# Performance work log

Measured on AMD Instinct MI355X. Metric: run time of the kernel, lower is better.

## Reference

```python
import jax, jax.numpy as jnp
import numpy as np

B, D, H, DM, O = 8192, 512, 1024, 2048, 256


def setup_inputs() -> dict:
    key = jax.random.key(0)
    ks = jax.random.split(key, 24)
    def rn(k, shape, scale=1.0):
        return jax.random.normal(k, shape, dtype=jnp.float32) * scale
    w = 0.02  # weight init scale
    return {
        "x":  rn(ks[0], (B, D)),
        "h0": rn(ks[1], (B, H), 0.1), "h1": rn(ks[2], (B, H), 0.1),
        "c0": rn(ks[3], (B, H), 0.1), "c1": rn(ks[4], (B, H), 0.1),
        # Bernoulli keep masks with model_prob=1.0 -> all ones
        "m0": jnp.ones((B, H), jnp.float32), "m1": jnp.ones((B, H), jnp.float32),
        # layer 0 gate weights: in = D + H = 1536
        "Wf0": rn(ks[5], (D + H, H), w), "bf0": jnp.full((H,), 0.01, jnp.float32),
        "Wi0": rn(ks[6], (D + H, H), w), "bi0": jnp.full((H,), 0.01, jnp.float32),
        "Wc0": rn(ks[7], (D + H, H), w), "bc0": jnp.full((H,), 0.01, jnp.float32),
        "Wo0": rn(ks[8], (D + H, H), w), "bo0": jnp.full((H,), 0.01, jnp.float32),
        # layer 1 gate weights: in = H + H = 2048
        "Wf1": rn(ks[9],  (2 * H, H), w), "bf1": jnp.full((H,), 0.01, jnp.float32),
        "Wi1": rn(ks[10], (2 * H, H), w), "bi1": jnp.full((H,), 0.01, jnp.float32),
        "Wc1": rn(ks[11], (2 * H, H), w), "bc1": jnp.full((H,), 0.01, jnp.float32),
        "Wo1": rn(ks[12], (2 * H, H), w), "bo1": jnp.full((H,), 0.01, jnp.float32),
        # output MLP: H -> DM -> O (identity activation per default nn.Sequential())
        "Wm1": rn(ks[13], (H, DM), w), "bm1": jnp.full((DM,), 0.01, jnp.float32),
        "Wm2": rn(ks[14], (DM, O), w), "bm2": jnp.full((O,), 0.01, jnp.float32),
    }


def _lstm_cell(comb, c, Wf, bf, Wi, bi, Wc, bc, Wo, bo):
    # fuse the 4 gate GEMMs into one matmul, then split
    W = jnp.concatenate([Wf, Wi, Wc, Wo], axis=1)      # [in, 4H]
    b = jnp.concatenate([bf, bi, bc, bo])               # [4H]
    g = comb @ W + b                                    # [B, 4H]
    f, i, ct, o = jnp.split(g, 4, axis=1)
    c_new = jax.nn.sigmoid(f) * c + jax.nn.sigmoid(i) * jnp.tanh(ct)
    h_new = jax.nn.sigmoid(o) * jnp.tanh(c_new)
    return h_new, c_new


def reference(x, h0, h1, c0, c1, m0, m1,
              Wf0, bf0, Wi0, bi0, Wc0, bc0, Wo0, bo0,
              Wf1, bf1, Wi1, bi1, Wc1, bc1, Wo1, bo1,
              Wm1, bm1, Wm2, bm2):
    # layer 0: combined = cat(input, h0 * mask0)
    comb0 = jnp.concatenate([x, h0 * m0], axis=1)       # [B, D+H]
    h0n, c0n = _lstm_cell(comb0, c0, Wf0, bf0, Wi0, bi0, Wc0, bc0, Wo0, bo0)
    # layer 1: combined = cat(h0_new * mask0, h1 * mask1)
    comb1 = jnp.concatenate([h0n * m0, h1 * m1], axis=1)  # [B, 2H]
    h1n, c1n = _lstm_cell(comb1, c1, Wf1, bf1, Wi1, bi1, Wc1, bc1, Wo1, bo1)
    # output MLP (dropout p=0 is identity; activation is identity Sequential)
    out = (h1n @ Wm1 + bm1) @ Wm2 + bm2                 # [B, O]
    return out, h0n, h1n, c0n, c1n
```

## Files before the change

### kernel.cpp

```cpp
#include <hip/hip_runtime.h>
#include <hip/hip_bf16.h>
#include <cstdint>
#include <cstddef>

#define DI __device__ __forceinline__

typedef __attribute__((ext_vector_type(8))) short short8;
typedef __attribute__((ext_vector_type(4))) float f32x4;

static constexpr int Bb = 8192, Dd = 512, Hh = 1024;

DI short f2b(float f) {
  union { __hip_bfloat16 h; short s; } u;
  u.h = __float2bfloat16(f);
  return u.s;
}

DI float sigm(float x) {
  float e = __builtin_amdgcn_exp2f(-1.4426950408889634f * x);
  return __builtin_amdgcn_rcpf(1.0f + e);
}
DI float tanh_(float x) {
  float xc = fminf(fmaxf(x, -20.0f), 20.0f);
  float e = __builtin_amdgcn_exp2f(-2.8853900817779268f * xc);
  return (1.0f - e) * __builtin_amdgcn_rcpf(1.0f + e);
}

DI void gload16(const void* g, void* l) {
  __builtin_amdgcn_global_load_lds(
      (const __attribute__((address_space(1))) uint32_t*)g,
      (__attribute__((address_space(3))) uint32_t*)l, 16, 0, 0);
}


__global__ void conv_A0(const float* __restrict__ x, const float* __restrict__ h0,
                        const float* __restrict__ m0, short* __restrict__ A0) {
  const int row = blockIdx.x, t = threadIdx.x;
  float v[8];
  if (t < 64) {
    const float4* p = (const float4*)(x + (size_t)row * Dd + t * 8);
    float4 a = p[0], b = p[1];
    v[0] = a.x; v[1] = a.y; v[2] = a.z; v[3] = a.w;
    v[4] = b.x; v[5] = b.y; v[6] = b.z; v[7] = b.w;
  } else {
    const int j = t * 8 - 512;
    const float4* ph = (const float4*)(h0 + (size_t)row * Hh + j);
    const float4* pm = (const float4*)(m0 + (size_t)row * Hh + j);
    float4 a = ph[0], b = ph[1], ma = pm[0], mb = pm[1];
    v[0] = a.x * ma.x; v[1] = a.y * ma.y; v[2] = a.z * ma.z; v[3] = a.w * ma.w;
    v[4] = b.x * mb.x; v[5] = b.y * mb.y; v[6] = b.z * mb.z; v[7] = b.w * mb.w;
  }
  short8 o;
  #pragma unroll
  for (int q = 0; q < 8; q++) o[q] = f2b(v[q]);
  *(short8*)(A0 + (size_t)row * 1536 + t * 8) = o;
}

__global__ void conv_A1hi(const float* __restrict__ h1, const float* __restrict__ m1,
                          short* __restrict__ A1) {
  const int row = blockIdx.x, t = threadIdx.x;
  const int j = t * 8;
  const float4* ph = (const float4*)(h1 + (size_t)row * Hh + j);
  const float4* pm = (const float4*)(m1 + (size_t)row * Hh + j);
  float4 a = ph[0], b = ph[1], ma = pm[0], mb = pm[1];
  float v[8] = {a.x * ma.x, a.y * ma.y, a.z * ma.z, a.w * ma.w,
                b.x * mb.x, b.y * mb.y, b.z * mb.z, b.w * mb.w};
  short8 o;
  #pragma unroll
  for (int q = 0; q < 8; q++) o[q] = f2b(v[q]);
  *(short8*)(A1 + (size_t)row * 2048 + 1024 + j) = o;
}

__global__ void transpose_conv(const float* __restrict__ src, short* __restrict__ dst,
                               int N, int K, int g, int interleave) {
  __shared__ float t[64][65];
  const int k0 = blockIdx.x * 64, n0 = blockIdx.y * 64;
  const int tid = threadIdx.x;
  const int r = tid >> 2, c0 = (tid & 3) * 16;
  const float* s = src + (size_t)(k0 + r) * N + n0 + c0;
  #pragma unroll
  for (int q = 0; q < 16; q += 4) {
    float4 v = *(const float4*)(s + q);
    t[r][c0 + q + 0] = v.x; t[r][c0 + q + 1] = v.y;
    t[r][c0 + q + 2] = v.z; t[r][c0 + q + 3] = v.w;
  }
  __syncthreads();
  const int n = n0 + r;
  const int j = interleave ? ((n >> 4) * 64 + g * 16 + (n & 15)) : n;
  short8 o0, o1;
  #pragma unroll
  for (int q = 0; q < 8; q++) o0[q] = f2b(t[c0 + q][r]);
  #pragma unroll
  for (int q = 0; q < 8; q++) o1[q] = f2b(t[c0 + 8 + q][r]);
  short* d = dst + (size_t)j * K + k0 + c0;
  *(short8*)d = o0;
  *((short8*)d + 1) = o1;
}

__global__ void conv_plain(const float* __restrict__ src, short* __restrict__ dst, int n8) {
  const int id = blockIdx.x * blockDim.x + threadIdx.x;
  if (id >= n8) return;
  const float4* p = (const float4*)(src + (size_t)id * 8);
  float4 a = p[0], b = p[1];
  short8 o;
  o[0] = f2b(a.x); o[1] = f2b(a.y); o[2] = f2b(a.z); o[3] = f2b(a.w);
  o[4] = f2b(b.x); o[5] = f2b(b.y); o[6] = f2b(b.z); o[7] = f2b(b.w);
  *(short8*)(dst + (size_t)id * 8) = o;
}

__global__ void bp_init(const float* __restrict__ bm2, float* __restrict__ bp) {
  bp[threadIdx.x] = bm2[threadIdx.x];
}
__global__ void bp_acc(const float* __restrict__ bm1, const float* __restrict__ Wm2,
                       float* __restrict__ bp) {
  const int o = threadIdx.x;
  const int k0 = blockIdx.x * 64;
  float s = 0.f;
  #pragma unroll 4
  for (int k = 0; k < 64; k++) s += bm1[k0 + k] * Wm2[(size_t)(k0 + k) * 256 + o];
  atomicAdd(&bp[o], s);
}

template <int EPI>
__global__ __launch_bounds__(256) void gemm_bt(
    const short* __restrict__ A, const short* __restrict__ Bt, int K,
    short* __restrict__ Cb, int ldc,
    float* __restrict__ outp, const float* __restrict__ bpv) {
  __shared__ __align__(16) short sA[128 * 32];
  __shared__ __align__(16) short sB[128 * 32];
  const int tid = threadIdx.x;
  const int lane = tid & 63;
  const int wave = tid >> 6;
  const int wm = wave >> 1, wn = wave & 1;
  const int bm = blockIdx.x, bn = blockIdx.y;
  const int lr = lane & 15, lq = lane >> 4;

  f32x4 acc[4][4] = {};

  const short* pA = A + ((size_t)(bm * 128 + (tid >> 2))) * K + (tid & 3) * 8;
  const short* pB = Bt + ((size_t)(bn * 128 + (tid >> 2))) * K + (tid & 3) * 8;
  short* lA = sA + tid * 8;
  short* lB = sB + tid * 8;
  const int aoff = (wm * 64 + lr) * 32 + lq * 8;
  const int boff = (wn * 64 + lr) * 32 + lq * 8;

  for (int k0 = 0; k0 < K; k0 += 32) {
    gload16(pA + k0, lA);
    gload16(pA + (size_t)64 * K + k0, lA + 2048);
    gload16(pB + k0, lB);
    gload16(pB + (size_t)64 * K + k0, lB + 2048);
    __syncthreads();
    short8 af[4], bv[4];
    #pragma unroll
    for (int m = 0; m < 4; m++) af[m] = *(const short8*)&sA[aoff + m * 512];
    #pragma unroll
    for (int n = 0; n < 4; n++) bv[n] = *(const short8*)&sB[boff + n * 512];
    #pragma unroll
    for (int m = 0; m < 4; m++)
      #pragma unroll
      for (int n = 0; n < 4; n++)
        acc[m][n] = __builtin_amdgcn_mfma_f32_16x16x32_bf16(af[m], bv[n], acc[m][n], 0, 0, 0);
    __syncthreads();
  }

  const int crow0 = bm * 128 + wm * 64 + lq * 4;
  const int ccol0 = bn * 128 + wn * 64 + lr;

  if constexpr (EPI == 0) {
    #pragma unroll
    for (int m = 0; m < 4; m++)
      #pragma unroll
      for (int r = 0; r < 4; r++) {
        const int row = crow0 + m * 16 + r;
        #pragma unroll
        for (int n = 0; n < 4; n++)
          Cb[(size_t)row * ldc + ccol0 + n * 16] = f2b(acc[m][n][r]);
      }
  } else {
    float bvv[4];
    #pragma unroll
    for (int n = 0; n < 4; n++) bvv[n] = bpv[ccol0 + n * 16];
    #pragma unroll
    for (int m = 0; m < 4; m++)
      #pragma unroll
      for (int r = 0; r < 4; r++) {
        const int row = crow0 + m * 16 + r;
        #pragma unroll
        for (int n = 0; n < 4; n++)
          outp[(size_t)row * 256 + ccol0 + n * 16] = acc[m][n][r] + bvv[n];
      }
  }
}


#define STA(buf, h, kt) { const short* s_ = gA + (size_t)(h) * 64 * K + (size_t)(kt) * 64; \
    gload16(s_ + aS0, &sA[buf][h][tid * 8]);                                               \
    gload16(s_ + aS1, &sA[buf][h][4096 + tid * 8]); }
#define STB(buf, h, kt) { const short* s_ = gB + (size_t)(h) * 128 * K + (size_t)(kt) * 64; \
    gload16(s_ + bS0, &sB[buf][h][tid * 8]);                                                \
    gload16(s_ + bS1, &sB[buf][h][4096 + tid * 8]); }

#define LDB(buf) {                                                \
    const short* bb = &sB[buf][bh][brb];                          \
    _Pragma("unroll") for (int n = 0; n < 4; n++) {               \
      bv[n][0] = *(const short8*)(bb + n * 1024 + sw0);           \
      bv[n][1] = *(const short8*)(bb + n * 1024 + sw1); } }

#define LDA_(buf, q, av) {                                        \
    const short* ab = &sA[buf][(q) >> 1][arb + ((q) & 1) * 2048]; \
    av[0][0] = *(const short8*)(ab + sw0);                        \
    av[0][1] = *(const short8*)(ab + sw1);                        \
    av[1][0] = *(const short8*)(ab + 1024 + sw0);                 \
    av[1][1] = *(const short8*)(ab + 1024 + sw1); }

#define MM(q, av) {                                               \
    __builtin_amdgcn_s_setprio(1);                                \
    _Pragma("unroll") for (int m = 0; m < 2; m++)                 \
    _Pragma("unroll") for (int n = 0; n < 4; n++) {               \
      acc[2*(q)+m][n] = __builtin_amdgcn_mfma_f32_16x16x32_bf16(av[m][0], bv[n][0], acc[2*(q)+m][n], 0, 0, 0); \
      acc[2*(q)+m][n] = __builtin_amdgcn_mfma_f32_16x16x32_bf16(av[m][1], bv[n][1], acc[2*(q)+m][n], 0, 0, 0); } \
    __builtin_amdgcn_s_setprio(0); }

#define BAR() asm volatile("s_barrier" ::: "memory")
#define VM6() asm volatile("s_waitcnt vmcnt(6)" ::: "memory")

#define PH(buf, q, STG, vm) { short8 av[2][2]; LDA_(buf, q, av); STG; \
    if (vm) VM6(); BAR(); MM(q, av); BAR(); }

__global__ __launch_bounds__(512, 2) void gemm8_lstm(
    const short* __restrict__ A, const short* __restrict__ Bt, const int K,
    const float* __restrict__ cprev, float* __restrict__ hout,
    float* __restrict__ cout, short* __restrict__ anext, const int ldan,
    const float* __restrict__ mask,
    const float* __restrict__ bF, const float* __restrict__ bI,
    const float* __restrict__ bC, const float* __restrict__ bO) {
  __shared__ __align__(16) short sA[2][2][8192];
  __shared__ __align__(16) short sB[2][2][8192];
  const int tid = threadIdx.x;
  const int lane = tid & 63, wid = tid >> 6;
  const int wr = wid >> 2, wc = wid & 3;
  const int lr = lane & 15, lq = lane >> 4;

  const int wgf = blockIdx.y * 32 + blockIdx.x;
  const int swz = (wgf & 7) * 64 + (wgf >> 3);
  const int bm = swz & 31;
  const int bn = swz >> 5;

  const int NT = K >> 6;
  const int NIT = NT >> 1;

  const int r0 = tid >> 3;
  const int csw = (tid & 7) ^ (r0 & 7);
  const int growA0 = ((r0 >> 5) & 1) * 32 + (r0 & 31);
  const int growA1 = 128 + growA0;
  const size_t aS0 = (size_t)growA0 * K + csw * 8;
  const size_t aS1 = (size_t)growA1 * K + csw * 8;
  const size_t bS0 = (size_t)r0 * K + csw * 8;
  const size_t bS1 = (size_t)(r0 + 64) * K + csw * 8;
  const short* gA = A + (size_t)bm * 256 * K;
  const short* gB = Bt + (size_t)bn * 256 * K;

  const int arb = (wr * 64 + lr) * 64;
  const int brb = ((wc & 1) * 64 + lr) * 64;
  const int bh = wc >> 1;
  const int sw0 = ((lq) ^ (lr & 7)) * 8;
  const int sw1 = ((4 + lq) ^ (lr & 7)) * 8;

  f32x4 acc[8][4] = {};
  short8 bv[4][2];

  STB(0, 0, 0); STB(0, 1, 0); STA(0, 0, 0); STA(0, 1, 0);
  STB(1, 0, 1); STB(1, 1, 1); STA(1, 0, 1);
  VM6(); BAR();

  for (int it = 0; it < NIT; ++it) {
    const int k1 = 2 * it + 1;
    int t2 = 2 * it + 2; if (t2 >= NT) t2 = 0;
    int t3 = 2 * it + 3; if (t3 >= NT) t3 = 1;
    { short8 av[2][2]; LDB(0); LDA_(0, 0, av); STA(1, 1, k1); BAR(); MM(0, av); BAR(); }
    PH(0, 1, STB(0, 0, t2), 0);
    PH(0, 2, STB(0, 1, t2), 0);
    PH(0, 3, STA(0, 0, t2), 1);
    { short8 av[2][2]; LDB(1); LDA_(1, 0, av); STA(0, 1, t2); BAR(); MM(0, av); BAR(); }
    PH(1, 1, STB(1, 0, t3), 0);
    PH(1, 2, STB(1, 1, t3), 0);
    PH(1, 3, STA(1, 0, t3), 1);
  }

  const int n = (bn * 4 + wc) * 16 + lr;
  const float bf_ = bF[n], bi_ = bI[n], bc_ = bC[n], bo_ = bO[n];
  const int row0 = bm * 256 + wr * 128 + lq * 4;

  float cp[4], mk[4], cpn[4], mkn[4];
  #pragma unroll
  for (int rr = 0; rr < 4; rr++) {
    const size_t idx = (size_t)(row0 + rr) * 1024 + n;
    cp[rr] = cprev[idx];
    mk[rr] = mask ? mask[idx] : 1.0f;
  }
  #pragma unroll
  for (int mf = 0; mf < 8; mf++) {
    if (mf < 7) {
      #pragma unroll
      for (int rr = 0; rr < 4; rr++) {
        const size_t idx2 = (size_t)(row0 + (mf + 1) * 16 + rr) * 1024 + n;
        cpn[rr] = cprev[idx2];
        mkn[rr] = mask ? mask[idx2] : 1.0f;
      }
    }
    #pragma unroll
    for (int rr = 0; rr < 4; rr++) {
      const int row = row0 + mf * 16 + rr;
      const size_t idx = (size_t)row * 1024 + n;
      const float fg = sigm(acc[mf][0][rr] + bf_);
      const float ig = sigm(acc[mf][1][rr] + bi_);
      const float cg = tanh_(acc[mf][2][rr] + bc_);
      const float og = sigm(acc[mf][3][rr] + bo_);
      const float cn = fg * cp[rr] + ig * cg;
      const float hn = og * tanh_(cn);
      cout[idx] = cn;
      hout[idx] = hn;
      anext[(size_t)row * ldan + n] = f2b(hn * mk[rr]);
    }
    #pragma unroll
    for (int rr = 0; rr < 4; rr++) { cp[rr] = cpn[rr]; mk[rr] = mkn[rr]; }
  }
}


extern "C" void kernel_launch(void* const* d_in, const int* in_sizes, int n_in,
                              void* d_out, int out_size, void* d_ws, size_t ws_size,
                              hipStream_t stream) {
  (void)in_sizes; (void)n_in; (void)out_size; (void)ws_size;
  const float* x   = (const float*)d_in[0];
  const float* h0  = (const float*)d_in[1];
  const float* h1  = (const float*)d_in[2];
  const float* c0  = (const float*)d_in[3];
  const float* c1  = (const float*)d_in[4];
  const float* m0  = (const float*)d_in[5];
  const float* m1  = (const float*)d_in[6];
  const float* Wf0 = (const float*)d_in[7];  const float* bf0 = (const float*)d_in[8];
  const float* Wi0 = (const float*)d_in[9];  const float* bi0 = (const float*)d_in[10];
  const float* Wc0 = (const float*)d_in[11]; const float* bc0 = (const float*)d_in[12];
  const float* Wo0 = (const float*)d_in[13]; const float* bo0 = (const float*)d_in[14];
  const float* Wf1 = (const float*)d_in[15]; const float* bf1 = (const float*)d_in[16];
  const float* Wi1 = (const float*)d_in[17]; const float* bi1 = (const float*)d_in[18];
  const float* Wc1 = (const float*)d_in[19]; const float* bc1 = (const float*)d_in[20];
  const float* Wo1 = (const float*)d_in[21]; const float* bo1 = (const float*)d_in[22];
  const float* Wm1 = (const float*)d_in[23]; const float* bm1 = (const float*)d_in[24];
  const float* Wm2 = (const float*)d_in[25]; const float* bm2 = (const float*)d_in[26];

  float* dout  = (float*)d_out;
  float* out_o = dout;
  float* h0n   = dout + 2097152;
  float* h1n   = h0n + 8388608;
  float* c0n   = h1n + 8388608;
  float* c1n   = c0n + 8388608;

  char* ws = (char*)d_ws;
  short* A0   = (short*)(ws);
  short* A1   = (short*)(ws + 25165824);
  short* A2   = (short*)(ws + 58720256);
  short* WT0  = (short*)(ws + 75497472);
  short* WT1  = (short*)(ws + 88080384);
  short* Wm1b = (short*)(ws + 104857600);
  short* Wm2T = (short*)(ws + 109051904);
  short* WpT  = (short*)(ws + 110100480);
  float* bp   = (float*)(ws + 110624768);

  conv_A0<<<dim3(8192), dim3(192), 0, stream>>>(x, h0, m0, A0);
  conv_A1hi<<<dim3(8192), dim3(128), 0, stream>>>(h1, m1, A1);
  transpose_conv<<<dim3(24, 16), dim3(256), 0, stream>>>(Wf0, WT0, 1024, 1536, 0, 1);
  transpose_conv<<<dim3(24, 16), dim3(256), 0, stream>>>(Wi0, WT0, 1024, 1536, 1, 1);
  transpose_conv<<<dim3(24, 16), dim3(256), 0, stream>>>(Wc0, WT0, 1024, 1536, 2, 1);
  transpose_conv<<<dim3(24, 16), dim3(256), 0, stream>>>(Wo0, WT0, 1024, 1536, 3, 1);
  transpose_conv<<<dim3(32, 16), dim3(256), 0, stream>>>(Wf1, WT1, 1024, 2048, 0, 1);
  transpose_conv<<<dim3(32, 16), dim3(256), 0, stream>>>(Wi1, WT1, 1024, 2048, 1, 1);
  transpose_conv<<<dim3(32, 16), dim3(256), 0, stream>>>(Wc1, WT1, 1024, 2048, 2, 1);
  transpose_conv<<<dim3(32, 16), dim3(256), 0, stream>>>(Wo1, WT1, 1024, 2048, 3, 1);
  conv_plain<<<dim3(1024), dim3(256), 0, stream>>>(Wm1, Wm1b, 262144);
  transpose_conv<<<dim3(32, 4), dim3(256), 0, stream>>>(Wm2, Wm2T, 256, 2048, 0, 0);
  bp_init<<<dim3(1), dim3(256), 0, stream>>>(bm2, bp);
  bp_acc<<<dim3(32), dim3(256), 0, stream>>>(bm1, Wm2, bp);

  gemm_bt<0><<<dim3(2, 8), dim3(256), 0, stream>>>(
      Wm2T, Wm1b, 2048, WpT, 1024, nullptr, nullptr);

  gemm8_lstm<<<dim3(32, 16), dim3(512), 0, stream>>>(
      A0, WT0, 1536, c0, h0n, c0n, A1, 2048, m0, bf0, bi0, bc0, bo0);

  gemm8_lstm<<<dim3(32, 16), dim3(512), 0, stream>>>(
      A1, WT1, 2048, c1, h1n, c1n, A2, 1024, nullptr, bf1, bi1, bc1, bo1);

  gemm_bt<1><<<dim3(64, 2), dim3(256), 0, stream>>>(
      A2, WpT, 1024, nullptr, 0, out_o, bp);
}
```

Baseline: 409.3 us.

## Batch gate-weight transposes into single launches and drop LSTM GEMM block swizzle

Replaces eight per-gate weight transpose launches with two launches that use a z grid dimension to select the gate, cutting launch overhead and small-grid tail effects. The LSTM GEMM kernel also drops its workgroup-index swizzle and maps blockIdx directly to tile row and column, which changes L2 reuse of A and B tiles across concurrently running blocks. The swizzle removal may reduce cache locality.

```diff
diff --git a/kernel.cpp b/kernel.cpp
--- a/kernel.cpp
+++ b/kernel.cpp
@@ -71,8 +71,37 @@
   *(short8*)(A1 + (size_t)row * 2048 + 1024 + j) = o;
 }
 
+__global__ void transpose_conv4(const float* __restrict__ s0, const float* __restrict__ s1,
+                                const float* __restrict__ s2, const float* __restrict__ s3,
+                                short* __restrict__ dst, int N, int K) {
+  __shared__ float t[64][65];
+  const int g = blockIdx.z;
+  const float* src = (g == 0) ? s0 : (g == 1) ? s1 : (g == 2) ? s2 : s3;
+  const int k0 = blockIdx.x * 64, n0 = blockIdx.y * 64;
+  const int tid = threadIdx.x;
+  const int r = tid >> 2, c0 = (tid & 3) * 16;
+  const float* s = src + (size_t)(k0 + r) * N + n0 + c0;
+  #pragma unroll
+  for (int q = 0; q < 16; q += 4) {
+    float4 v = *(const float4*)(s + q);
+    t[r][c0 + q + 0] = v.x; t[r][c0 + q + 1] = v.y;
+    t[r][c0 + q + 2] = v.z; t[r][c0 + q + 3] = v.w;
+  }
+  __syncthreads();
+  const int n = n0 + r;
+  const int j = (n >> 4) * 64 + g * 16 + (n & 15);
+  short8 o0, o1;
+  #pragma unroll
+  for (int q = 0; q < 8; q++) o0[q] = f2b(t[c0 + q][r]);
+  #pragma unroll
+  for (int q = 0; q < 8; q++) o1[q] = f2b(t[c0 + 8 + q][r]);
+  short* d = dst + (size_t)j * K + k0 + c0;
+  *(short8*)d = o0;
+  *((short8*)d + 1) = o1;
+}
+
 __global__ void transpose_conv(const float* __restrict__ src, short* __restrict__ dst,
-                               int N, int K, int g, int interleave) {
+                               int N, int K) {
   __shared__ float t[64][65];
   const int k0 = blockIdx.x * 64, n0 = blockIdx.y * 64;
   const int tid = threadIdx.x;
@@ -86,13 +115,12 @@
   }
   __syncthreads();
   const int n = n0 + r;
-  const int j = interleave ? ((n >> 4) * 64 + g * 16 + (n & 15)) : n;
   short8 o0, o1;
   #pragma unroll
   for (int q = 0; q < 8; q++) o0[q] = f2b(t[c0 + q][r]);
   #pragma unroll
   for (int q = 0; q < 8; q++) o1[q] = f2b(t[c0 + 8 + q][r]);
-  short* d = dst + (size_t)j * K + k0 + c0;
+  short* d = dst + (size_t)n * K + k0 + c0;
   *(short8*)d = o0;
   *((short8*)d + 1) = o1;
 }
@@ -241,10 +269,7 @@
   const int wr = wid >> 2, wc = wid & 3;
   const int lr = lane & 15, lq = lane >> 4;
 
-  const int wgf = blockIdx.y * 32 + blockIdx.x;
-  const int swz = (wgf & 7) * 64 + (wgf >> 3);
-  const int bm = swz & 31;
-  const int bn = swz >> 5;
+  const int bm = blockIdx.x, bn = blockIdx.y;
 
   const int NT = K >> 6;
   const int NIT = NT >> 1;
@@ -370,16 +395,10 @@
 
   conv_A0<<<dim3(8192), dim3(192), 0, stream>>>(x, h0, m0, A0);
   conv_A1hi<<<dim3(8192), dim3(128), 0, stream>>>(h1, m1, A1);
-  transpose_conv<<<dim3(24, 16), dim3(256), 0, stream>>>(Wf0, WT0, 1024, 1536, 0, 1);
-  transpose_conv<<<dim3(24, 16), dim3(256), 0, stream>>>(Wi0, WT0, 1024, 1536, 1, 1);
-  transpose_conv<<<dim3(24, 16), dim3(256), 0, stream>>>(Wc0, WT0, 1024, 1536, 2, 1);
-  transpose_conv<<<dim3(24, 16), dim3(256), 0, stream>>>(Wo0, WT0, 1024, 1536, 3, 1);
-  transpose_conv<<<dim3(32, 16), dim3(256), 0, stream>>>(Wf1, WT1, 1024, 2048, 0, 1);
-  transpose_conv<<<dim3(32, 16), dim3(256), 0, stream>>>(Wi1, WT1, 1024, 2048, 1, 1);
-  transpose_conv<<<dim3(32, 16), dim3(256), 0, stream>>>(Wc1, WT1, 1024, 2048, 2, 1);
-  transpose_conv<<<dim3(32, 16), dim3(256), 0, stream>>>(Wo1, WT1, 1024, 2048, 3, 1);
+  transpose_conv4<<<dim3(24, 16, 4), dim3(256), 0, stream>>>(Wf0, Wi0, Wc0, Wo0, WT0, 1024, 1536);
+  transpose_conv4<<<dim3(32, 16, 4), dim3(256), 0, stream>>>(Wf1, Wi1, Wc1, Wo1, WT1, 1024, 2048);
   conv_plain<<<dim3(1024), dim3(256), 0, stream>>>(Wm1, Wm1b, 262144);
-  transpose_conv<<<dim3(32, 4), dim3(256), 0, stream>>>(Wm2, Wm2T, 256, 2048, 0, 0);
+  transpose_conv<<<dim3(32, 4), dim3(256), 0, stream>>>(Wm2, Wm2T, 256, 2048);
   bp_init<<<dim3(1), dim3(256), 0, stream>>>(bm2, bp);
   bp_acc<<<dim3(32), dim3(256), 0, stream>>>(bm1, Wm2, bp);
 
```

Result: faster. 392.5 us (-4.1%).
